# Kernel optimization log

Measured on AMD Instinct MI355X. Metric: run time of the kernel, lower is better.

## Reference

```python
import jax, jax.numpy as jnp
import numpy as np

B = 4
H32, W32 = 10, 32  # x_blocks[-1] spatial size (320x1024 input, stride 32)


def _conv3x3(x, w, b, mode):
    # Conv3x3: explicit pad (zero / reflect / edge==replicate) then VALID 3x3 conv
    if mode == 'zero':
        xp = jnp.pad(x, ((0, 0), (0, 0), (1, 1), (1, 1)))
    else:
        xp = jnp.pad(x, ((0, 0), (0, 0), (1, 1), (1, 1)), mode=mode)
    y = jax.lax.conv_general_dilated(xp, w, (1, 1), 'VALID',
                                     dimension_numbers=('NCHW', 'OIHW', 'NCHW'))
    return y + b[None, :, None, None]


def _maxpool(x, k):
    # nn.MaxPool2d(k, stride=1, padding=k//2)
    return jax.lax.reduce_window(x, -jnp.inf, jax.lax.max,
                                 (1, 1, k, k), (1, 1, 1, 1), 'SAME')


def _up2x(x):
    return jnp.repeat(jnp.repeat(x, 2, axis=2), 2, axis=3)


def _idwt_haar(ll, lh, hl, hh):
    # single-level inverse Haar DWT (orthonormal); pad mode irrelevant for length-2 filters
    b, c, h, w = ll.shape
    x00 = (ll + lh + hl + hh) * 0.5
    x01 = (ll - lh + hl - hh) * 0.5
    x10 = (ll + lh - hl - hh) * 0.5
    x11 = (ll - lh - hl + hh) * 0.5
    top = jnp.stack([x00, x01], axis=4).reshape(b, c, h, 2 * w)
    bot = jnp.stack([x10, x11], axis=4).reshape(b, c, h, 2 * w)
    return jnp.stack([top, bot], axis=3).reshape(b, c, 2 * h, 2 * w)


def _leaky(x):
    return jax.nn.leaky_relu(x, 0.2)


def setup_inputs():
    key = jax.random.key(0)
    ks = jax.random.split(key, 24)
    f = 1104  # int(2208 * 0.5)

    def w(k, o, i):
        return jax.random.normal(k, (o, i, 3, 3), jnp.float32) * (1.0 / np.sqrt(9.0 * i))

    def bs(k, o):
        return jax.random.normal(k, (o,), jnp.float32) * 0.01

    return {
        'x32': jax.random.normal(ks[0], (B, 2208, H32, W32), jnp.float32),
        'x16': jax.random.normal(ks[1], (B, 384, 2 * H32, 2 * W32), jnp.float32),
        'x8': jax.random.normal(ks[2], (B, 192, 4 * H32, 4 * W32), jnp.float32),
        'x4': jax.random.normal(ks[3], (B, 96, 8 * H32, 8 * W32), jnp.float32),
        'conv2_w': w(ks[4], f, 2208), 'conv2_b': bs(ks[5], f),
        'up1_w': w(ks[6], f // 2, f + 384), 'up1_b': bs(ks[7], f // 2),
        'wave1ll_w': w(ks[8], 1, f // 2), 'wave1ll_b': bs(ks[9], 1),
        'wave1_w': w(ks[10], 3, f // 2), 'wave1_b': bs(ks[11], 3),
        'up2_w': w(ks[12], f // 4, f // 2 + 192), 'up2_b': bs(ks[13], f // 4),
        'wave2_w': w(ks[14], 3, f // 4), 'wave2_b': bs(ks[15], 3),
        'up3_w': w(ks[16], f // 8, f // 4 + 96), 'up3_b': bs(ks[17], f // 8),
        'wave3_w': w(ks[18], 3, f // 8), 'wave3_b': bs(ks[19], 3),
    }


def reference(x32, x16, x8, x4, conv2_w, conv2_b, up1_w, up1_b,
              wave1ll_w, wave1ll_b, wave1_w, wave1_b, up2_w, up2_b,
              wave2_w, wave2_b, up3_w, up3_b, wave3_w, wave3_b):
    tr = 0.1  # thresh_ratio default
    # dense stem
    x_d0 = _conv3x3(x32, conv2_w, conv2_b, 'edge')  # replicate pad
    x_d1 = _leaky(_conv3x3(jnp.concatenate([_up2x(x_d0), x16], 1), up1_w, up1_b, 'reflect'))
    ll = 8.0 * _conv3x3(x_d1, wave1ll_w, wave1ll_b, 'edge')   # 2**3 * LL, [B,1,20,64]
    h = 4.0 * _conv3x3(x_d1, wave1_w, wave1_b, 'zero')        # 2**2 * (LH,HL,HH)
    ll = _idwt_haar(ll, h[:, 0:1], h[:, 1:2], h[:, 2:3])       # [B,1,40,128]

    # --- sparse level 1: dense-equivalent gather-compute-scatter via masks ---
    thresh = (ll.max() - ll.min()) * tr
    mask = (jnp.max(jnp.abs(h), axis=1, keepdims=True) > thresh).astype(jnp.float32)
    up_m = (_maxpool(mask, 5) > 0).astype(jnp.float32)
    conva_m = (_maxpool(_up2x(mask), 5) > 0).astype(jnp.float32)
    wave_m = (_maxpool(_up2x(mask), 3) > 0).astype(jnp.float32)
    wavelet_m = _up2x(mask)
    feat = jnp.concatenate([_up2x(x_d1 * up_m), x8], 1) * conva_m
    xa = _leaky(_conv3x3(feat, up2_w, up2_b, 'reflect')) * wave_m
    h = 2.0 * _conv3x3(xa, wave2_w, wave2_b, 'zero') * wavelet_m
    ll = _idwt_haar(ll, h[:, 0:1], h[:, 1:2], h[:, 2:3])       # [B,1,80,256]

    # --- sparse level 0 ---
    thresh = (ll.max() - ll.min()) * tr
    mask = (jnp.max(jnp.abs(h), axis=1, keepdims=True) > thresh).astype(jnp.float32)
    up_m = (_maxpool(mask, 5) > 0).astype(jnp.float32)
    conva_m = (_maxpool(_up2x(mask), 5) > 0).astype(jnp.float32)
    wave_m = (_maxpool(_up2x(mask), 3) > 0).astype(jnp.float32)
    wavelet_m = _up2x(mask)
    feat = jnp.concatenate([_up2x(xa * up_m), x4], 1) * conva_m  # sparse_select + sparse_upsample
    xb = _leaky(_conv3x3(feat, up3_w, up3_b, 'reflect')) * wave_m
    h = _conv3x3(xb, wave3_w, wave3_b, 'zero') * wavelet_m
    ll = _idwt_haar(ll, h[:, 0:1], h[:, 1:2], h[:, 2:3])       # [B,1,160,512]
    return ll  # outputs['disp', 0]
```

## Files before the change

kernel.cpp:

```cpp
#include <hip/hip_runtime.h>
#include <hip/hip_bf16.h>
#include <stdint.h>


typedef float f32x4 __attribute__((ext_vector_type(4)));
typedef short s16x8 __attribute__((ext_vector_type(8)));

__device__ __forceinline__ ushort f2bf(float f) {
    uint32_t u = __float_as_uint(f);
    u += 0x7FFFu + ((u >> 16) & 1u);
    return (ushort)(u >> 16);
}
__device__ __forceinline__ float bf2f(ushort h) {
    return __uint_as_float(((uint32_t)h) << 16);
}

__global__ __launch_bounds__(256)
void repack_w_k(const float* __restrict__ w, ushort* __restrict__ out,
                int OC, int CT, int ICOFF, int CAR, int CAP, int CAT,
                int CBR, int CBP, int SEG, int OCP, int KT)
{
    const int KG = KT / 8;
    const int u = blockIdx.x * 256 + threadIdx.x;
    if (u >= OCP * KG) return;
    const int oc = u / KG, kg = u - oc * KG;
    const int k0 = kg * 8;
    int ic, lo; bool ok;
    if (k0 < SEG * CAP) {
        const int seg = k0 / CAP, c = k0 - seg * CAP;
        lo = (seg == 2); ic = ICOFF + c; ok = (c < CAR);
    } else {
        const int kb = k0 - SEG * CAP;
        const int seg = kb / CBP, c = kb - seg * CBP;
        lo = (seg == 2); ic = CAT + c; ok = (c < CBR);
    }
    ok = ok && (oc < OC);
    for (int t = 0; t < 9; ++t) {
        ushort q[8];
#pragma unroll
        for (int j = 0; j < 8; ++j) q[j] = 0;
        if (ok) {
#pragma unroll
            for (int j = 0; j < 8; ++j) {
                const float v = w[((size_t)oc * CT + ic + j) * 9 + t];
                const ushort h = f2bf(v);
                q[j] = lo ? f2bf(v - bf2f(h)) : h;
            }
        }
        *(uint4*)(out + ((size_t)t * OCP + oc) * KT + k0) = *(uint4*)q;
    }
}

template<bool SPLIT>
__global__ __launch_bounds__(256)
void repack_x_k(const float* __restrict__ in, ushort* __restrict__ out,
                int C, int HW, int OST, int LOOFF)
{
    __shared__ float tile[32][65];
    const int b = blockIdx.z, c0 = blockIdx.y * 32, p0 = blockIdx.x * 64;
    for (int e = threadIdx.x; e < 2048; e += 256) {
        const int cl = e >> 6, pl = e & 63;
        tile[cl][pl] = in[((size_t)b * C + c0 + cl) * HW + p0 + pl];
    }
    __syncthreads();
    const int pl = threadIdx.x >> 2, cg = (threadIdx.x & 3) * 8;
    ushort hv[8], lv[8];
#pragma unroll
    for (int j = 0; j < 8; ++j) {
        const float v = tile[cg + j][pl];
        const ushort h = f2bf(v);
        hv[j] = h;
        lv[j] = f2bf(v - bf2f(h));
    }
    const size_t o = ((size_t)b * HW + p0 + pl) * OST + c0 + cg;
    *(uint4*)(out + o) = *(uint4*)hv;
    if constexpr (SPLIT) *(uint4*)(out + LOOFF + o) = *(uint4*)lv;
}

template<int MODE, int WR, int WC, int WROWS, int WCOLF, int NOCF,
         int H, int W, int OCP, int KT, int CAP, int CBP, int SEG,
         int ASTR, int APLSTR, int AOFF, int CAR, int BSTR, int KS,
         bool SOUT, bool ACCIN>
__global__ __launch_bounds__(256, 1)
void conv_mfma_k(const ushort* __restrict__ xA, const ushort* __restrict__ xB,
                 const ushort* __restrict__ wgt, const float* __restrict__ bias,
                 const float* __restrict__ upm, const float* __restrict__ cam,
                 const float* __restrict__ wvm,
                 ushort* __restrict__ outb, float* __restrict__ outp, int OC)
{
    constexpr int BROWS = WR * WROWS;
    constexpr int NOC = NOCF * 16;
    constexpr int PH = BROWS + 2, PW = 34;
    constexpr int NPX = PH * PW;
    constexpr int ICS = 32;
    constexpr int WRS = 32;
    constexpr int NAU = NPX * 4;
    constexpr int NWU = 9 * NOC * 4;
    constexpr int NSA = (NAU + 255) / 256;
    constexpr int NSW = (NWU + 255) / 256;
    constexpr int NCH = KT / 32;
    constexpr int XT = W / 32;
    constexpr int HP = ((H + BROWS - 1) / BROWS) * BROWS;
    constexpr int HA = (MODE == 0) ? H : H / 2;
    constexpr int WA = (MODE == 0) ? W : W / 2;

    __shared__ __align__(16) ushort atile[NPX * ICS];
    __shared__ __align__(16) ushort wtile[9 * NOC * WRS];

    const int tid = threadIdx.x;
    const int b = blockIdx.z / KS, sid = blockIdx.z % KS;
    const int oc0 = blockIdx.y * NOC;
    const int y0 = (blockIdx.x / XT) * BROWS;
    const int x0 = (blockIdx.x % XT) * 32;
    const int lane = tid & 63, wv = tid >> 6;
    const int wr = wv / WC, wc = wv % WC;
    const int lq = lane >> 4, ln = lane & 15;
    const int wcb = wc * (WCOLF * 16);

    const int c0 = (sid * NCH) / KS, c1 = ((sid + 1) * NCH) / KS;

    int aBA[NSA], aBB[NSA], aLD[NSA], aKO[NSA];
    bool agA[NSA], agB[NSA];
    for (int s = 0; s < NSA; ++s) {
        const int u = tid + s * 256;
        const bool val = u < NAU;
        const int uc = val ? u : 0;
        const int pp = uc >> 2, ug = uc & 3;
        const int py = pp / PW, px = pp - py * PW;
        int y = y0 + py - 1, x = x0 + px - 1;
        if (MODE == 0) { y = min(max(y, 0), H - 1); x = min(max(x, 0), W - 1); }
        else { y = (y < 0) ? -y : ((y >= H) ? 2 * H - 2 - y : y);
               x = (x < 0) ? -x : ((x >= W) ? 2 * W - 2 - x : x); }
        const int ya = (MODE == 0) ? y : (y >> 1);
        const int xa = (MODE == 0) ? x : (x >> 1);
        aBA[s] = ((b * HA + ya) * WA + xa) * ASTR;
        aBB[s] = ((b * H + y) * W + x) * BSTR;
        agA[s] = val; agB[s] = val;
        if (MODE == 2) {
            const float cm = cam[((size_t)b * H + y) * W + x];
            const float um = upm[((size_t)b * HA + ya) * WA + xa];
            agA[s] = agA[s] && (um * cm != 0.f);
            agB[s] = agB[s] && (cm != 0.f);
        }
        aLD[s] = pp * ICS + ((ug ^ ((pp >> 1) & 3)) * 8);
        aKO[s] = ug * 8;
    }
    int wGB[NSW], wLD[NSW]; bool wVv[NSW];
    for (int s = 0; s < NSW; ++s) {
        const int u = tid + s * 256;
        wVv[s] = u < NWU;
        const int uc = wVv[s] ? u : 0;
        const int t = uc / (NOC * 4), r = uc - t * (NOC * 4);
        const int ocl = r >> 2, kg = r & 3;
        const int wrow = t * NOC + ocl;
        wGB[s] = (t * OCP + oc0 + ocl) * KT + kg * 8;
        wLD[s] = wrow * WRS + ((kg ^ ((wrow >> 1) & 3)) * 8);
    }

    uint4 ra[NSA], rw[NSW];
    auto fetch = [&](int kc) {
#pragma unroll
        for (int s = 0; s < NSA; ++s) {
            const int k = kc * 32 + aKO[s];
            uint4 v = {0, 0, 0, 0};
            if (k < SEG * CAP) {
                int ka = (SEG == 3 && k >= 2 * CAP) ? k - 2 * CAP : k;
                const int pl = (ka >= CAP) ? 1 : 0;
                const int c = ka - pl * CAP;
                bool ok = agA[s];
                if (CAR < CAP) ok = ok && (c < CAR);
                if (ok) v = *(const uint4*)(xA + (size_t)aBA[s] + pl * APLSTR + AOFF + c);
            } else {
                int kb = k - SEG * CAP;
                if (SEG == 3 && kb >= 2 * CBP) kb -= 2 * CBP;
                if (agB[s]) v = *(const uint4*)(xB + (size_t)aBB[s] + kb);
            }
            ra[s] = v;
        }
#pragma unroll
        for (int s = 0; s < NSW; ++s) {
            uint4 v = {0, 0, 0, 0};
            if (wVv[s]) v = *(const uint4*)(wgt + (size_t)wGB[s] + kc * 32);
            rw[s] = v;
        }
    };
    auto put = [&]() {
#pragma unroll
        for (int s = 0; s < NSA; ++s)
            if (tid + s * 256 < NAU) *(uint4*)&atile[aLD[s]] = ra[s];
#pragma unroll
        for (int s = 0; s < NSW; ++s)
            if (wVv[s]) *(uint4*)&wtile[wLD[s]] = rw[s];
    };

    f32x4 acc[WROWS][WCOLF][NOCF];
#pragma unroll
    for (int i = 0; i < WROWS; ++i)
#pragma unroll
        for (int c = 0; c < WCOLF; ++c)
#pragma unroll
            for (int n = 0; n < NOCF; ++n) acc[i][c][n] = {0.f, 0.f, 0.f, 0.f};

    if (ACCIN) {
#pragma unroll
        for (int ri = 0; ri < WROWS; ++ri) {
            const float* Pr = outp +
                ((((size_t)sid * 4 + b) * HP + y0 + wr * WROWS + ri) * W + x0 + wcb) * OCP;
#pragma unroll
            for (int cf = 0; cf < WCOLF; ++cf)
#pragma unroll
                for (int n2 = 0; n2 < NOCF; ++n2)
#pragma unroll
                    for (int r = 0; r < 4; ++r)
                        acc[ri][cf][n2][r] =
                            Pr[(size_t)(cf * 16 + lq * 4 + r) * OCP + oc0 + n2 * 16 + ln];
        }
    }

    fetch(c0);
    put();
    __syncthreads();

    for (int kc = c0; kc < c1; ++kc) {
        const bool hn = (kc + 1 < c1);
        if (hn) fetch(kc + 1);
        s16x8 afr[WROWS + 2][WCOLF][3];
#pragma unroll
        for (int ar = 0; ar < WROWS + 2; ++ar)
#pragma unroll
            for (int cf = 0; cf < WCOLF; ++cf)
#pragma unroll
                for (int dx = 0; dx < 3; ++dx) {
                    const int p = (wr * WROWS + ar) * PW + wcb + cf * 16 + ln + dx;
                    afr[ar][cf][dx] = *(const s16x8*)
                        &atile[p * ICS + ((lq ^ ((p >> 1) & 3)) * 8)];
                }
#pragma unroll
        for (int t = 0; t < 9; ++t) {
            const int dy = t / 3, dx = t - dy * 3;
#pragma unroll
            for (int n2 = 0; n2 < NOCF; ++n2) {
                const int wrow = t * NOC + n2 * 16 + ln;
                const s16x8 bw = *(const s16x8*)
                    &wtile[wrow * WRS + ((lq ^ ((wrow >> 1) & 3)) * 8)];
#pragma unroll
                for (int ri = 0; ri < WROWS; ++ri)
#pragma unroll
                    for (int cf = 0; cf < WCOLF; ++cf)
                        acc[ri][cf][n2] = __builtin_amdgcn_mfma_f32_16x16x32_bf16(
                            afr[ri + dy][cf][dx], bw, acc[ri][cf][n2], 0, 0, 0);
            }
        }
        __syncthreads();
        if (hn) { put(); __syncthreads(); }
    }

    if (KS > 1) {
#pragma unroll
        for (int ri = 0; ri < WROWS; ++ri) {
            float* Pr = outp +
                ((((size_t)sid * 4 + b) * HP + y0 + wr * WROWS + ri) * W + x0 + wcb) * OCP;
#pragma unroll
            for (int cf = 0; cf < WCOLF; ++cf)
#pragma unroll
                for (int n2 = 0; n2 < NOCF; ++n2)
#pragma unroll
                    for (int r = 0; r < 4; ++r)
                        Pr[(size_t)(cf * 16 + lq * 4 + r) * OCP + oc0 + n2 * 16 + ln] =
                            acc[ri][cf][n2][r];
        }
    } else {
        constexpr int OST = SOUT ? 2 * OCP : OCP;
#pragma unroll
        for (int ri = 0; ri < WROWS; ++ri) {
            const int y = y0 + wr * WROWS + ri;
#pragma unroll
            for (int cf = 0; cf < WCOLF; ++cf)
#pragma unroll
                for (int n2 = 0; n2 < NOCF; ++n2) {
                    const int oc = oc0 + n2 * 16 + ln;
                    const float bv = (oc < OC) ? bias[oc] : 0.f;
#pragma unroll
                    for (int r = 0; r < 4; ++r) {
                        const int x = x0 + wcb + cf * 16 + lq * 4 + r;
                        float v = acc[ri][cf][n2][r] + bv;
                        v = v > 0.f ? v : 0.2f * v;
                        v *= wvm[((size_t)b * H + y) * W + x];
                        if (oc >= OC) v = 0.f;
                        const size_t o = (((size_t)b * H + y) * W + x) * OST + oc;
                        const ushort h = f2bf(v);
                        outb[o] = h;
                        if constexpr (SOUT) outb[o + OCP] = f2bf(v - bf2f(h));
                    }
                }
        }
    }
}

template<int KS, int HP, int H, int W, int OCP, bool ACT>
__global__ __launch_bounds__(256)
void reduce_k(const float* __restrict__ P, const float* __restrict__ bias,
              ushort* __restrict__ out, int OC)
{
    constexpr int OG = OCP / 4;
    const int u = blockIdx.x * 256 + threadIdx.x;
    if (u >= 4 * H * W * OG) return;
    const int og = u % OG;
    const int px = u / OG;
    const int x = px % W, y = (px / W) % H, b = px / (W * H);
    float4 s = {0.f, 0.f, 0.f, 0.f};
    for (int sid = 0; sid < KS; ++sid) {
        const float4 v = *(const float4*)
            (P + ((((size_t)sid * 4 + b) * HP + y) * W + x) * OCP + og * 4);
        s.x += v.x; s.y += v.y; s.z += v.z; s.w += v.w;
    }
    const int oc = og * 4;
    const float vv[4] = {s.x, s.y, s.z, s.w};
    ushort hi[4], lo[4];
#pragma unroll
    for (int j = 0; j < 4; ++j) {
        float v = (oc + j < OC) ? vv[j] + bias[oc + j] : 0.f;
        if (ACT) v = v > 0.f ? v : 0.2f * v;
        const ushort h = f2bf(v);
        hi[j] = h;
        lo[j] = f2bf(v - bf2f(h));
    }
    const size_t o = (size_t)px * 2 * OCP + oc;
    *(uint2*)(out + o) = *(uint2*)hi;
    *(uint2*)(out + o + OCP) = *(uint2*)lo;
}

__global__ __launch_bounds__(256)
void repack_wv_k(const float* __restrict__ wh, const float* __restrict__ wll,
                 float* __restrict__ out, int C, int CP)
{
    const int u = blockIdx.x * 256 + threadIdx.x;
    if (u >= 9 * CP) return;
    const int t = u / CP, ic = u - t * CP;
    float4 v = {0.f, 0.f, 0.f, 0.f};
    if (ic < C) {
        v.x = wh[((size_t)0 * C + ic) * 9 + t];
        v.y = wh[((size_t)1 * C + ic) * 9 + t];
        v.z = wh[((size_t)2 * C + ic) * 9 + t];
        if (wll) v.w = wll[(size_t)ic * 9 + t];
    }
    *(float4*)(out + (size_t)u * 4) = v;
}

template<int G, int CSTR, int LOOFF, int H, int W, bool SIN, bool HAS_LL>
__global__ __launch_bounds__(256)
void wave_cl_k(const ushort* __restrict__ xq, const float* __restrict__ wv,
               const float* __restrict__ bh, const float* __restrict__ bll,
               const float* __restrict__ mhalf, float scale,
               float* __restrict__ outh, float* __restrict__ outll)
{
    const int lane = threadIdx.x & 63;
    const int pix = blockIdx.x * 4 + (threadIdx.x >> 6);
    const int x = pix % W, y = (pix / W) % H, b = pix / (W * H);
    float a0 = 0.f, a1 = 0.f, a2 = 0.f, a3 = 0.f;
    for (int it = lane; it < 9 * G; it += 64) {
        const int t = it / G, g = it - t * G;
        const int dy = t / 3 - 1, dx = t % 3 - 1;
        const int yy = y + dy, xx = x + dx;
        const int yc = min(max(yy, 0), H - 1), xc = min(max(xx, 0), W - 1);
        const bool inr = (yy >= 0) && (yy < H) && (xx >= 0) && (xx < W);
        const size_t base = (((size_t)b * H + yc) * W + xc) * CSTR + g * 8;
        const uint4 hv = *(const uint4*)(xq + base);
        uint4 lv = {0, 0, 0, 0};
        if constexpr (!SIN) lv = *(const uint4*)(xq + base + LOOFF);
        const float4* wp = (const float4*)(wv + ((size_t)t * (G * 8) + g * 8) * 4);
        const uint* hw = (const uint*)&hv;
        const uint* lw = (const uint*)&lv;
#pragma unroll
        for (int j = 0; j < 8; ++j) {
            const uint wd = hw[j >> 1];
            float xf = (j & 1) ? __uint_as_float(wd & 0xFFFF0000u)
                               : __uint_as_float(wd << 16);
            if constexpr (!SIN) {
                const uint wl = lw[j >> 1];
                xf += (j & 1) ? __uint_as_float(wl & 0xFFFF0000u)
                              : __uint_as_float(wl << 16);
            }
            const float xz = inr ? xf : 0.f;
            const float4 w4 = wp[j];
            a0 = fmaf(w4.x, xz, a0);
            a1 = fmaf(w4.y, xz, a1);
            a2 = fmaf(w4.z, xz, a2);
            if constexpr (HAS_LL) a3 = fmaf(w4.w, xf, a3);
        }
    }
#pragma unroll
    for (int o = 1; o < 64; o <<= 1) {
        a0 += __shfl_xor(a0, o);
        a1 += __shfl_xor(a1, o);
        a2 += __shfl_xor(a2, o);
        if constexpr (HAS_LL) a3 += __shfl_xor(a3, o);
    }
    if (lane == 0) {
        float wm = 1.f;
        if (mhalf) wm = mhalf[((size_t)b * (H / 2) + (y >> 1)) * (W / 2) + (x >> 1)];
        const size_t hb = (size_t)b * 3 * H * W + (size_t)y * W + x;
        outh[hb]             = (a0 + bh[0]) * scale * wm;
        outh[hb + H * W]     = (a1 + bh[1]) * scale * wm;
        outh[hb + 2 * H * W] = (a2 + bh[2]) * scale * wm;
        if constexpr (HAS_LL) outll[((size_t)b * H + y) * W + x] = (a3 + bll[0]) * 8.f;
    }
}

template<int H, int W>
__global__ __launch_bounds__(256)
void idwt_k(const float* __restrict__ ll, const float* __restrict__ h,
            float* __restrict__ out)
{
    const int g = blockIdx.x * 256 + threadIdx.x;
    if (g >= 4 * H * W) return;
    const int x = g % W, y = (g / W) % H, b = g / (W * H);
    const float l  = ll[g];
    const float lh = h[((size_t)(b * 3 + 0) * H + y) * W + x];
    const float hl = h[((size_t)(b * 3 + 1) * H + y) * W + x];
    const float hh = h[((size_t)(b * 3 + 2) * H + y) * W + x];
    const float x00 = (l + lh + hl + hh) * 0.5f;
    const float x01 = (l - lh + hl - hh) * 0.5f;
    const float x10 = (l + lh - hl - hh) * 0.5f;
    const float x11 = (l - lh - hl + hh) * 0.5f;
    float* ob = out + (size_t)b * (2 * H) * (2 * W);
    ob[(size_t)(2 * y) * (2 * W) + 2 * x]         = x00;
    ob[(size_t)(2 * y) * (2 * W) + 2 * x + 1]     = x01;
    ob[(size_t)(2 * y + 1) * (2 * W) + 2 * x]     = x10;
    ob[(size_t)(2 * y + 1) * (2 * W) + 2 * x + 1] = x11;
}

__global__ __launch_bounds__(256)
void minmax_k(const float* __restrict__ p, int n, float* __restrict__ thr)
{
    __shared__ float smax[256], smin[256];
    float mx = -1e30f, mn = 1e30f;
    for (int i = threadIdx.x; i < n; i += 256) {
        const float v = p[i];
        mx = fmaxf(mx, v);
        mn = fminf(mn, v);
    }
    smax[threadIdx.x] = mx;
    smin[threadIdx.x] = mn;
    __syncthreads();
    for (int s = 128; s > 0; s >>= 1) {
        if (threadIdx.x < s) {
            smax[threadIdx.x] = fmaxf(smax[threadIdx.x], smax[threadIdx.x + s]);
            smin[threadIdx.x] = fminf(smin[threadIdx.x], smin[threadIdx.x + s]);
        }
        __syncthreads();
    }
    if (threadIdx.x == 0) *thr = (smax[0] - smin[0]) * 0.1f;
}

template<int H, int W>
__global__ __launch_bounds__(256)
void mask_k(const float* __restrict__ h, const float* __restrict__ thr,
            float* __restrict__ mask)
{
    const int g = blockIdx.x * 256 + threadIdx.x;
    if (g >= 4 * H * W) return;
    const int x = g % W, y = (g / W) % H, b = g / (W * H);
    const float t  = *thr;
    const float v0 = fabsf(h[((size_t)(b * 3 + 0) * H + y) * W + x]);
    const float v1 = fabsf(h[((size_t)(b * 3 + 1) * H + y) * W + x]);
    const float v2 = fabsf(h[((size_t)(b * 3 + 2) * H + y) * W + x]);
    mask[g] = (fmaxf(v0, fmaxf(v1, v2)) > t) ? 1.f : 0.f;
}

template<int H, int W, int R>
__global__ __launch_bounds__(256)
void dilate_k(const float* __restrict__ m, float* __restrict__ o)
{
    const int g = blockIdx.x * 256 + threadIdx.x;
    if (g >= 4 * H * W) return;
    const int x = g % W, y = (g / W) % H, b = g / (W * H);
    float v = 0.f;
    for (int dy = -R; dy <= R; ++dy) {
        const int yy = y + dy;
        if (yy < 0 || yy >= H) continue;
        for (int dx = -R; dx <= R; ++dx) {
            const int xx = x + dx;
            if (xx < 0 || xx >= W) continue;
            v = fmaxf(v, m[((size_t)b * H + yy) * W + xx]);
        }
    }
    o[g] = (v > 0.f) ? 1.f : 0.f;
}

template<int H, int W>
__global__ __launch_bounds__(256)
void masksfull_k(const float* __restrict__ m, float* __restrict__ conva,
                 float* __restrict__ wavem)
{
    const int g = blockIdx.x * 256 + threadIdx.x;
    constexpr int H2 = 2 * H, W2 = 2 * W;
    if (g >= 4 * H2 * W2) return;
    const int x = g % W2, y = (g / W2) % H2, b = g / (W2 * H2);
    float c5 = 0.f, c3 = 0.f;
    for (int dy = -2; dy <= 2; ++dy) {
        const int yy = y + dy;
        if (yy < 0 || yy >= H2) continue;
        const int my = yy >> 1;
        for (int dx = -2; dx <= 2; ++dx) {
            const int xx = x + dx;
            if (xx < 0 || xx >= W2) continue;
            const float v = m[((size_t)b * H + my) * W + (xx >> 1)];
            c5 = fmaxf(c5, v);
            if (dy >= -1 && dy <= 1 && dx >= -1 && dx <= 1) c3 = fmaxf(c3, v);
        }
    }
    conva[g] = (c5 > 0.f) ? 1.f : 0.f;
    wavem[g] = (c3 > 0.f) ? 1.f : 0.f;
}

static constexpr size_t WSTEM = 0;
static constexpr size_t WUP1  = 0;
static constexpr size_t X16   = 46780416ull;
static constexpr size_t WUP2  = 54644736ull;
static constexpr size_t XB    = 0ull;
static constexpr size_t X4    = 23592960ull;
static constexpr size_t WUP3  = 66769920ull;
static constexpr size_t WV1   = 67765248ull;
static constexpr size_t WV2   = 67844736ull;
static constexpr size_t WV3   = 67885056ull;
static constexpr size_t X32   = 66769920ull;
static constexpr size_t XD0   = 78074880ull;
static constexpr size_t PF    = 83727360ull;
static constexpr size_t XAOF  = 83727360ull;
static constexpr size_t XD1   = 110859264ull;
static constexpr size_t X8    = 122655744ull;
static constexpr size_t F32B  = 138384384ull;
static constexpr size_t O_LL1 = 0, O_H1 = 5120, O_LLB = 20480, O_H2 = 40960;
static constexpr size_t O_LLC = 102400, O_H3 = 184320, O_M1 = 430080;
static constexpr size_t O_UPM1 = 435200, O_CAM1 = 440320, O_WM1 = 460800;
static constexpr size_t O_M2 = 481280, O_UPM2 = 501760, O_CAM2 = 522240;
static constexpr size_t O_WM2 = 604160, O_RED = 686080;

extern "C" void kernel_launch(void* const* d_in, const int* in_sizes, int n_in,
                              void* d_out, int out_size, void* d_ws, size_t ws_size,
                              hipStream_t stream)
{
    const float* x32     = (const float*)d_in[0];
    const float* x16     = (const float*)d_in[1];
    const float* x8      = (const float*)d_in[2];
    const float* x4      = (const float*)d_in[3];
    const float* conv2_w = (const float*)d_in[4];
    const float* conv2_b = (const float*)d_in[5];
    const float* up1_w   = (const float*)d_in[6];
    const float* up1_b   = (const float*)d_in[7];
    const float* w1ll_w  = (const float*)d_in[8];
    const float* w1ll_b  = (const float*)d_in[9];
    const float* w1_w    = (const float*)d_in[10];
    const float* w1_b    = (const float*)d_in[11];
    const float* up2_w   = (const float*)d_in[12];
    const float* up2_b   = (const float*)d_in[13];
    const float* w2_w    = (const float*)d_in[14];
    const float* w2_b    = (const float*)d_in[15];
    const float* up3_w   = (const float*)d_in[16];
    const float* up3_b   = (const float*)d_in[17];
    const float* w3_w    = (const float*)d_in[18];
    const float* w3_b    = (const float*)d_in[19];

    char* ws = (char*)d_ws;
    auto U = [&](size_t off) { return (ushort*)(ws + off); };
    float* Pf  = (float*)(ws + PF);
    float* f32 = (float*)(ws + F32B);
    float* ll1   = f32 + O_LL1;
    float* h1    = f32 + O_H1;
    float* llb   = f32 + O_LLB;
    float* h2    = f32 + O_H2;
    float* llc   = f32 + O_LLC;
    float* h3    = f32 + O_H3;
    float* mask1 = f32 + O_M1;
    float* upm1  = f32 + O_UPM1;
    float* cam1  = f32 + O_CAM1;
    float* wm1   = f32 + O_WM1;
    float* mask2 = f32 + O_M2;
    float* upm2  = f32 + O_UPM2;
    float* cam2  = f32 + O_CAM2;
    float* wm2   = f32 + O_WM2;
    float* wv1   = (float*)(ws + WV1);
    float* wv2   = (float*)(ws + WV2);
    float* wv3   = (float*)(ws + WV3);

    repack_x_k<true><<<dim3(5, 69, 4), 256, 0, stream>>>(x32, U(X32), 2208, 320, 4416, 2208);
    repack_w_k<<<1812, 256, 0, stream>>>(conv2_w, U(WSTEM), 1104, 2208, 0, 1104, 1120, 0, 0, 8, 3, 1104, 3360);
    conv_mfma_k<0, 2, 2, 2, 1, 3, 10, 32, 1104, 3360, 1120, 8, 3, 4416, 2208, 0, 1104, 1, 4, false, false>
        <<<dim3(3, 23, 16), 256, 0, stream>>>(U(X32), nullptr, U(WSTEM), nullptr,
            nullptr, nullptr, nullptr, nullptr, Pf, 1104);
    repack_w_k<<<1812, 256, 0, stream>>>(conv2_w, U(WSTEM), 1104, 2208, 1104, 1104, 1120, 0, 0, 8, 3, 1104, 3360);
    conv_mfma_k<0, 2, 2, 2, 1, 3, 10, 32, 1104, 3360, 1120, 8, 3, 4416, 2208, 1104, 1104, 1, 4, false, true>
        <<<dim3(3, 23, 16), 256, 0, stream>>>(U(X32), nullptr, U(WSTEM), nullptr,
            nullptr, nullptr, nullptr, nullptr, Pf, 1104);
    reduce_k<4, 12, 10, 32, 1104, false><<<1380, 256, 0, stream>>>(Pf, conv2_b, U(XD0), 1104);
    repack_w_k<<<1269, 256, 0, stream>>>(up1_w, U(WUP1), 552, 1488, 0, 1104, 1120, 1104, 384, 384, 3, 576, 4512);
    repack_x_k<true><<<dim3(20, 12, 4), 256, 0, stream>>>(x16, U(X16), 384, 1280, 768, 384);
    repack_w_k<<<324, 256, 0, stream>>>(up2_w, U(WUP2), 276, 744, 0, 552, 576, 552, 192, 192, 3, 288, 2304);
    repack_w_k<<<27, 256, 0, stream>>>(up3_w, U(WUP3), 138, 372, 0, 276, 288, 276, 96, 96, 1, 144, 384);
    repack_x_k<true><<<dim3(80, 6, 4), 256, 0, stream>>>(x8, U(X8), 192, 5120, 384, 192);
    repack_wv_k<<<20, 256, 0, stream>>>(w1_w, w1ll_w, wv1, 552, 552);
    repack_wv_k<<<10, 256, 0, stream>>>(w2_w, nullptr, wv2, 276, 280);
    repack_wv_k<<<6, 256, 0, stream>>>(w3_w, nullptr, wv3, 138, 144);
    conv_mfma_k<1, 2, 2, 2, 1, 4, 20, 64, 576, 4512, 1120, 384, 3, 2208, 1104, 0, 1104, 768, 2, false, false>
        <<<dim3(10, 9, 8), 256, 0, stream>>>(U(XD0), U(X16), U(WUP1), nullptr,
            nullptr, nullptr, nullptr, nullptr, Pf, 552);
    reduce_k<2, 20, 20, 64, 576, true><<<2880, 256, 0, stream>>>(Pf, up1_b, U(XD1), 552);
    repack_x_k<false><<<dim3(320, 3, 4), 256, 0, stream>>>(x4, U(X4), 96, 20480, 96, 0);
    wave_cl_k<69, 1152, 576, 20, 64, false, true><<<1280, 256, 0, stream>>>(
        U(XD1), wv1, w1_b, w1ll_b, nullptr, 4.f, h1, ll1);
    idwt_k<20, 64><<<20, 256, 0, stream>>>(ll1, h1, llb);
    minmax_k<<<1, 256, 0, stream>>>(llb, 20480, f32 + O_RED);
    mask_k<20, 64><<<20, 256, 0, stream>>>(h1, f32 + O_RED, mask1);
    dilate_k<20, 64, 2><<<20, 256, 0, stream>>>(mask1, upm1);
    masksfull_k<20, 64><<<80, 256, 0, stream>>>(mask1, cam1, wm1);
    conv_mfma_k<2, 4, 1, 2, 2, 3, 40, 128, 288, 2304, 576, 192, 3, 1152, 576, 0, 576, 384, 1, true, false>
        <<<dim3(20, 6, 4), 256, 0, stream>>>(U(XD1), U(X8), U(WUP2), up2_b,
            upm1, cam1, wm1, U(XAOF), nullptr, 276);
    wave_cl_k<35, 576, 288, 40, 128, false, false><<<5120, 256, 0, stream>>>(
        U(XAOF), wv2, w2_b, nullptr, mask1, 2.f, h2, nullptr);
    idwt_k<40, 128><<<80, 256, 0, stream>>>(llb, h2, llc);
    minmax_k<<<1, 256, 0, stream>>>(llc, 81920, f32 + O_RED + 1);
    mask_k<40, 128><<<80, 256, 0, stream>>>(h2, f32 + O_RED + 1, mask2);
    dilate_k<40, 128, 2><<<80, 256, 0, stream>>>(mask2, upm2);
    masksfull_k<40, 128><<<320, 256, 0, stream>>>(mask2, cam2, wm2);
    conv_mfma_k<2, 4, 1, 2, 2, 3, 80, 256, 144, 384, 288, 96, 1, 576, 288, 0, 288, 96, 1, false, false>
        <<<dim3(80, 3, 4), 256, 0, stream>>>(U(XAOF), U(X4), U(WUP3), up3_b,
            upm2, cam2, wm2, U(XB), nullptr, 138);
    wave_cl_k<18, 144, 0, 80, 256, true, false><<<20480, 256, 0, stream>>>(
        U(XB), wv3, w3_b, nullptr, mask2, 1.f, h3, nullptr);
    idwt_k<80, 256><<<320, 256, 0, stream>>>(llc, h3, (float*)d_out);
}
```

Baseline: 2.558 ms.

## Double-buffer conv tiles with direct global-to-LDS async loads and retiled blocks

Replaces the register-staged fetch/put loop of the MFMA conv kernel with global_load_lds direct-to-LDS copies into two LDS buffers, so the next K-chunk loads while the current one computes and one barrier per iteration is dropped. Masked or out-of-range loads are redirected to a zeroed pad buffer instead of predicated zero writes, which needs a new zeroing kernel and a workspace shift. Block tiling, OC-per-block and launch bounds (2 blocks/CU) are retuned for each conv. The risk is LDS pressure and the lost CAR channel check, which now relies on zero-padded data, for example in the XD0 head.

After: 2.639 ms. +3.1%, slower.

```diff
diff --git a/kernel.cpp b/kernel.cpp
--- a/kernel.cpp
+++ b/kernel.cpp
@@ -5,6 +5,13 @@
 
 typedef float f32x4 __attribute__((ext_vector_type(4)));
 typedef short s16x8 __attribute__((ext_vector_type(8)));
+
+typedef const __attribute__((address_space(1))) void* gas_ptr;
+typedef __attribute__((address_space(3))) void* las_ptr;
+
+__device__ __forceinline__ void gl_lds16(const void* g, void* l) {
+    __builtin_amdgcn_global_load_lds((gas_ptr)g, (las_ptr)l, 16, 0, 0);
+}
 
 __device__ __forceinline__ ushort f2bf(float f) {
     uint32_t u = __float_as_uint(f);
@@ -13,6 +20,15 @@
 }
 __device__ __forceinline__ float bf2f(ushort h) {
     return __uint_as_float(((uint32_t)h) << 16);
+}
+
+__global__ __launch_bounds__(256)
+void zero_k(ushort* __restrict__ zp, ushort* __restrict__ xd0head)
+{
+    const int t = threadIdx.x;
+    const uint4 z = {0, 0, 0, 0};
+    for (int i = t; i < 1024; i += 256) *(uint4*)(zp + i * 8) = z;
+    if (t < 16) *(uint4*)(xd0head + t * 8) = z;
 }
 
 __global__ __launch_bounds__(256)
@@ -79,118 +95,109 @@
 
 template<int MODE, int WR, int WC, int WROWS, int WCOLF, int NOCF,
          int H, int W, int OCP, int KT, int CAP, int CBP, int SEG,
-         int ASTR, int APLSTR, int AOFF, int CAR, int BSTR, int KS,
+         int ASTR, int APLSTR, int AOFF, int BSTR, int KS,
          bool SOUT, bool ACCIN>
-__global__ __launch_bounds__(256, 1)
-void conv_mfma_k(const ushort* __restrict__ xA, const ushort* __restrict__ xB,
-                 const ushort* __restrict__ wgt, const float* __restrict__ bias,
-                 const float* __restrict__ upm, const float* __restrict__ cam,
-                 const float* __restrict__ wvm,
-                 ushort* __restrict__ outb, float* __restrict__ outp, int OC)
+__global__ __launch_bounds__(256, 2)
+void conv_async_k(const ushort* __restrict__ xA, const ushort* __restrict__ xB,
+                  const ushort* __restrict__ wgt, const float* __restrict__ bias,
+                  const float* __restrict__ upm, const float* __restrict__ cam,
+                  const float* __restrict__ wvm, const ushort* __restrict__ zpad,
+                  ushort* __restrict__ outb, float* __restrict__ outp, int OC)
 {
     constexpr int BROWS = WR * WROWS;
+    constexpr int BCOLS = WC * WCOLF * 16;
     constexpr int NOC = NOCF * 16;
-    constexpr int PH = BROWS + 2, PW = 34;
+    constexpr int PH = BROWS + 2, PW = BCOLS + 2;
     constexpr int NPX = PH * PW;
-    constexpr int ICS = 32;
-    constexpr int WRS = 32;
     constexpr int NAU = NPX * 4;
+    constexpr int ASL = ((NAU + 63) / 64) * 64;
     constexpr int NWU = 9 * NOC * 4;
-    constexpr int NSA = (NAU + 255) / 256;
+    constexpr int NSA = (ASL + 255) / 256;
     constexpr int NSW = (NWU + 255) / 256;
+    constexpr int PERBUF = (ASL + NWU) * 8;
     constexpr int NCH = KT / 32;
-    constexpr int XT = W / 32;
+    constexpr int XT = W / BCOLS;
     constexpr int HP = ((H + BROWS - 1) / BROWS) * BROWS;
     constexpr int HA = (MODE == 0) ? H : H / 2;
     constexpr int WA = (MODE == 0) ? W : W / 2;
-
-    __shared__ __align__(16) ushort atile[NPX * ICS];
-    __shared__ __align__(16) ushort wtile[9 * NOC * WRS];
+    constexpr bool HASB = (SEG * CAP < KT);
+
+    __shared__ __align__(16) ushort lds[2 * PERBUF];
 
     const int tid = threadIdx.x;
     const int b = blockIdx.z / KS, sid = blockIdx.z % KS;
     const int oc0 = blockIdx.y * NOC;
     const int y0 = (blockIdx.x / XT) * BROWS;
-    const int x0 = (blockIdx.x % XT) * 32;
+    const int x0 = (blockIdx.x % XT) * BCOLS;
     const int lane = tid & 63, wv = tid >> 6;
     const int wr = wv / WC, wc = wv % WC;
     const int lq = lane >> 4, ln = lane & 15;
     const int wcb = wc * (WCOLF * 16);
-
     const int c0 = (sid * NCH) / KS, c1 = ((sid + 1) * NCH) / KS;
-
-    int aBA[NSA], aBB[NSA], aLD[NSA], aKO[NSA];
-    bool agA[NSA], agB[NSA];
+    const int wbv = wv * 512;
+
+    const ushort* pAp[NSA]; const ushort* pBp[NSA]; int aKO[NSA];
     for (int s = 0; s < NSA; ++s) {
         const int u = tid + s * 256;
-        const bool val = u < NAU;
-        const int uc = val ? u : 0;
-        const int pp = uc >> 2, ug = uc & 3;
-        const int py = pp / PW, px = pp - py * PW;
+        const int pp = u >> 2, sl = u & 3;
+        aKO[s] = (sl ^ ((pp >> 1) & 3)) * 8;
+        const bool val = pp < NPX;
+        const int ppc = val ? pp : 0;
+        const int py = ppc / PW, px = ppc - py * PW;
         int y = y0 + py - 1, x = x0 + px - 1;
         if (MODE == 0) { y = min(max(y, 0), H - 1); x = min(max(x, 0), W - 1); }
         else { y = (y < 0) ? -y : ((y >= H) ? 2 * H - 2 - y : y);
                x = (x < 0) ? -x : ((x >= W) ? 2 * W - 2 - x : x); }
         const int ya = (MODE == 0) ? y : (y >> 1);
         const int xa = (MODE == 0) ? x : (x >> 1);
-        aBA[s] = ((b * HA + ya) * WA + xa) * ASTR;
-        aBB[s] = ((b * H + y) * W + x) * BSTR;
-        agA[s] = val; agB[s] = val;
+        bool okA = val, okB = val;
         if (MODE == 2) {
             const float cm = cam[((size_t)b * H + y) * W + x];
             const float um = upm[((size_t)b * HA + ya) * WA + xa];
-            agA[s] = agA[s] && (um * cm != 0.f);
-            agB[s] = agB[s] && (cm != 0.f);
-        }
-        aLD[s] = pp * ICS + ((ug ^ ((pp >> 1) & 3)) * 8);
-        aKO[s] = ug * 8;
-    }
-    int wGB[NSW], wLD[NSW]; bool wVv[NSW];
+            okA = okA && (um * cm != 0.f);
+            okB = okB && (cm != 0.f);
+        }
+        pAp[s] = okA ? xA + (size_t)((b * HA + ya) * WA + xa) * ASTR : zpad;
+        if constexpr (HASB)
+            pBp[s] = okB ? xB + (size_t)((b * H + y) * W + x) * BSTR : zpad;
+        else
+            pBp[s] = zpad;
+    }
+    const ushort* pWp[NSW];
     for (int s = 0; s < NSW; ++s) {
         const int u = tid + s * 256;
-        wVv[s] = u < NWU;
-        const int uc = wVv[s] ? u : 0;
-        const int t = uc / (NOC * 4), r = uc - t * (NOC * 4);
-        const int ocl = r >> 2, kg = r & 3;
-        const int wrow = t * NOC + ocl;
-        wGB[s] = (t * OCP + oc0 + ocl) * KT + kg * 8;
-        wLD[s] = wrow * WRS + ((kg ^ ((wrow >> 1) & 3)) * 8);
-    }
-
-    uint4 ra[NSA], rw[NSW];
-    auto fetch = [&](int kc) {
+        const int wrow = u >> 2, sl = u & 3;
+        const int kg = sl ^ ((wrow >> 1) & 3);
+        const int t = wrow / NOC, ocl = wrow - t * NOC;
+        pWp[s] = (u < NWU) ?
+            wgt + (size_t)(t * OCP + oc0 + ocl) * KT + kg * 8 : zpad;
+    }
+
+    auto stage = [&](int buf, int kc) {
+        ushort* ab = lds + buf * PERBUF;
+        ushort* wb = ab + ASL * 8;
+        const int ko = kc * 32;
 #pragma unroll
         for (int s = 0; s < NSA; ++s) {
-            const int k = kc * 32 + aKO[s];
-            uint4 v = {0, 0, 0, 0};
-            if (k < SEG * CAP) {
-                int ka = (SEG == 3 && k >= 2 * CAP) ? k - 2 * CAP : k;
-                const int pl = (ka >= CAP) ? 1 : 0;
-                const int c = ka - pl * CAP;
-                bool ok = agA[s];
-                if (CAR < CAP) ok = ok && (c < CAR);
-                if (ok) v = *(const uint4*)(xA + (size_t)aBA[s] + pl * APLSTR + AOFF + c);
-            } else {
-                int kb = k - SEG * CAP;
-                if (SEG == 3 && kb >= 2 * CBP) kb -= 2 * CBP;
-                if (agB[s]) v = *(const uint4*)(xB + (size_t)aBB[s] + kb);
+            if (s * 256 + wv * 64 < NAU) {
+                const int k = ko + aKO[s];
+                const ushort* g;
+                if (!HASB || k < SEG * CAP) {
+                    int ka = (SEG == 3 && k >= 2 * CAP) ? k - 2 * CAP : k;
+                    const int pl = (ka >= CAP) ? 1 : 0;
+                    g = pAp[s] + pl * APLSTR + AOFF + (ka - pl * CAP);
+                } else {
+                    int kb = k - SEG * CAP;
+                    if (SEG == 3 && kb >= 2 * CBP) kb -= 2 * CBP;
+                    g = pBp[s] + kb;
+                }
+                gl_lds16(g, ab + s * 2048 + wbv);
             }
-            ra[s] = v;
-        }
-#pragma unroll
-        for (int s = 0; s < NSW; ++s) {
-            uint4 v = {0, 0, 0, 0};
-            if (wVv[s]) v = *(const uint4*)(wgt + (size_t)wGB[s] + kc * 32);
-            rw[s] = v;
-        }
-    };
-    auto put = [&]() {
-#pragma unroll
-        for (int s = 0; s < NSA; ++s)
-            if (tid + s * 256 < NAU) *(uint4*)&atile[aLD[s]] = ra[s];
+        }
 #pragma unroll
         for (int s = 0; s < NSW; ++s)
-            if (wVv[s]) *(uint4*)&wtile[wLD[s]] = rw[s];
+            if (s * 256 + wv * 64 < NWU)
+                gl_lds16(pWp[s] + ko, wb + s * 2048 + wbv);
     };
 
     f32x4 acc[WROWS][WCOLF][NOCF];
@@ -217,13 +224,13 @@
         }
     }
 
-    fetch(c0);
-    put();
+    stage(0, c0);
     __syncthreads();
-
+    int cur = 0;
     for (int kc = c0; kc < c1; ++kc) {
-        const bool hn = (kc + 1 < c1);
-        if (hn) fetch(kc + 1);
+        if (kc + 1 < c1) stage(cur ^ 1, kc + 1);
+        const ushort* at = lds + cur * PERBUF;
+        const ushort* wt = at + ASL * 8;
         s16x8 afr[WROWS + 2][WCOLF][3];
 #pragma unroll
         for (int ar = 0; ar < WROWS + 2; ++ar)
@@ -233,7 +240,7 @@
                 for (int dx = 0; dx < 3; ++dx) {
                     const int p = (wr * WROWS + ar) * PW + wcb + cf * 16 + ln + dx;
                     afr[ar][cf][dx] = *(const s16x8*)
-                        &atile[p * ICS + ((lq ^ ((p >> 1) & 3)) * 8)];
+                        &at[p * 32 + ((lq ^ ((p >> 1) & 3)) * 8)];
                 }
 #pragma unroll
         for (int t = 0; t < 9; ++t) {
@@ -242,7 +249,7 @@
             for (int n2 = 0; n2 < NOCF; ++n2) {
                 const int wrow = t * NOC + n2 * 16 + ln;
                 const s16x8 bw = *(const s16x8*)
-                    &wtile[wrow * WRS + ((lq ^ ((wrow >> 1) & 3)) * 8)];
+                    &wt[wrow * 32 + ((lq ^ ((wrow >> 1) & 3)) * 8)];
 #pragma unroll
                 for (int ri = 0; ri < WROWS; ++ri)
 #pragma unroll
@@ -252,7 +259,7 @@
             }
         }
         __syncthreads();
-        if (hn) { put(); __syncthreads(); }
+        cur ^= 1;
     }
 
     if (KS > 1) {
@@ -526,8 +533,9 @@
 static constexpr size_t WV3   = 67885056ull;
 static constexpr size_t X32   = 66769920ull;
 static constexpr size_t XD0   = 78074880ull;
-static constexpr size_t PF    = 83727360ull;
-static constexpr size_t XAOF  = 83727360ull;
+static constexpr size_t ZPADO = 83727360ull;
+static constexpr size_t PF    = 83743744ull;
+static constexpr size_t XAOF  = 83743744ull;
 static constexpr size_t XD1   = 110859264ull;
 static constexpr size_t X8    = 122655744ull;
 static constexpr size_t F32B  = 138384384ull;
@@ -583,16 +591,19 @@
     float* wv1   = (float*)(ws + WV1);
     float* wv2   = (float*)(ws + WV2);
     float* wv3   = (float*)(ws + WV3);
+    const ushort* zp = U(ZPADO);
+
+    zero_k<<<1, 256, 0, stream>>>(U(ZPADO), U(XD0));
 
     repack_x_k<true><<<dim3(5, 69, 4), 256, 0, stream>>>(x32, U(X32), 2208, 320, 4416, 2208);
     repack_w_k<<<1812, 256, 0, stream>>>(conv2_w, U(WSTEM), 1104, 2208, 0, 1104, 1120, 0, 0, 8, 3, 1104, 3360);
-    conv_mfma_k<0, 2, 2, 2, 1, 3, 10, 32, 1104, 3360, 1120, 8, 3, 4416, 2208, 0, 1104, 1, 4, false, false>
-        <<<dim3(3, 23, 16), 256, 0, stream>>>(U(X32), nullptr, U(WSTEM), nullptr,
-            nullptr, nullptr, nullptr, nullptr, Pf, 1104);
+    conv_async_k<0, 4, 1, 1, 1, 3, 10, 32, 1104, 3360, 1120, 8, 3, 4416, 2208, 0, 1, 4, false, false>
+        <<<dim3(6, 23, 16), 256, 0, stream>>>(U(X32), nullptr, U(WSTEM), nullptr,
+            nullptr, nullptr, nullptr, zp, nullptr, Pf, 1104);
     repack_w_k<<<1812, 256, 0, stream>>>(conv2_w, U(WSTEM), 1104, 2208, 1104, 1104, 1120, 0, 0, 8, 3, 1104, 3360);
-    conv_mfma_k<0, 2, 2, 2, 1, 3, 10, 32, 1104, 3360, 1120, 8, 3, 4416, 2208, 1104, 1104, 1, 4, false, true>
-        <<<dim3(3, 23, 16), 256, 0, stream>>>(U(X32), nullptr, U(WSTEM), nullptr,
-            nullptr, nullptr, nullptr, nullptr, Pf, 1104);
+    conv_async_k<0, 4, 1, 1, 1, 3, 10, 32, 1104, 3360, 1120, 8, 3, 4416, 2208, 1104, 1, 4, false, true>
+        <<<dim3(6, 23, 16), 256, 0, stream>>>(U(X32), nullptr, U(WSTEM), nullptr,
+            nullptr, nullptr, nullptr, zp, nullptr, Pf, 1104);
     reduce_k<4, 12, 10, 32, 1104, false><<<1380, 256, 0, stream>>>(Pf, conv2_b, U(XD0), 1104);
     repack_w_k<<<1269, 256, 0, stream>>>(up1_w, U(WUP1), 552, 1488, 0, 1104, 1120, 1104, 384, 384, 3, 576, 4512);
     repack_x_k<true><<<dim3(20, 12, 4), 256, 0, stream>>>(x16, U(X16), 384, 1280, 768, 384);
@@ -602,9 +613,9 @@
     repack_wv_k<<<20, 256, 0, stream>>>(w1_w, w1ll_w, wv1, 552, 552);
     repack_wv_k<<<10, 256, 0, stream>>>(w2_w, nullptr, wv2, 276, 280);
     repack_wv_k<<<6, 256, 0, stream>>>(w3_w, nullptr, wv3, 138, 144);
-    conv_mfma_k<1, 2, 2, 2, 1, 4, 20, 64, 576, 4512, 1120, 384, 3, 2208, 1104, 0, 1104, 768, 2, false, false>
-        <<<dim3(10, 9, 8), 256, 0, stream>>>(U(XD0), U(X16), U(WUP1), nullptr,
-            nullptr, nullptr, nullptr, nullptr, Pf, 552);
+    conv_async_k<1, 2, 2, 2, 1, 2, 20, 64, 576, 4512, 1120, 384, 3, 2208, 1104, 0, 768, 2, false, false>
+        <<<dim3(10, 18, 8), 256, 0, stream>>>(U(XD0), U(X16), U(WUP1), nullptr,
+            nullptr, nullptr, nullptr, zp, nullptr, Pf, 552);
     reduce_k<2, 20, 20, 64, 576, true><<<2880, 256, 0, stream>>>(Pf, up1_b, U(XD1), 552);
     repack_x_k<false><<<dim3(320, 3, 4), 256, 0, stream>>>(x4, U(X4), 96, 20480, 96, 0);
     wave_cl_k<69, 1152, 576, 20, 64, false, true><<<1280, 256, 0, stream>>>(
@@ -614,9 +625,9 @@
     mask_k<20, 64><<<20, 256, 0, stream>>>(h1, f32 + O_RED, mask1);
     dilate_k<20, 64, 2><<<20, 256, 0, stream>>>(mask1, upm1);
     masksfull_k<20, 64><<<80, 256, 0, stream>>>(mask1, cam1, wm1);
-    conv_mfma_k<2, 4, 1, 2, 2, 3, 40, 128, 288, 2304, 576, 192, 3, 1152, 576, 0, 576, 384, 1, true, false>
-        <<<dim3(20, 6, 4), 256, 0, stream>>>(U(XD1), U(X8), U(WUP2), up2_b,
-            upm1, cam1, wm1, U(XAOF), nullptr, 276);
+    conv_async_k<2, 2, 2, 2, 1, 2, 40, 128, 288, 2304, 576, 192, 3, 1152, 576, 0, 384, 1, true, false>
+        <<<dim3(40, 9, 4), 256, 0, stream>>>(U(XD1), U(X8), U(WUP2), up2_b,
+            upm1, cam1, wm1, zp, U(XAOF), nullptr, 276);
     wave_cl_k<35, 576, 288, 40, 128, false, false><<<5120, 256, 0, stream>>>(
         U(XAOF), wv2, w2_b, nullptr, mask1, 2.f, h2, nullptr);
     idwt_k<40, 128><<<80, 256, 0, stream>>>(llb, h2, llc);
@@ -624,9 +635,9 @@
     mask_k<40, 128><<<80, 256, 0, stream>>>(h2, f32 + O_RED + 1, mask2);
     dilate_k<40, 128, 2><<<80, 256, 0, stream>>>(mask2, upm2);
     masksfull_k<40, 128><<<320, 256, 0, stream>>>(mask2, cam2, wm2);
-    conv_mfma_k<2, 4, 1, 2, 2, 3, 80, 256, 144, 384, 288, 96, 1, 576, 288, 0, 288, 96, 1, false, false>
-        <<<dim3(80, 3, 4), 256, 0, stream>>>(U(XAOF), U(X4), U(WUP3), up3_b,
-            upm2, cam2, wm2, U(XB), nullptr, 138);
+    conv_async_k<2, 2, 2, 2, 1, 1, 80, 256, 144, 384, 288, 96, 1, 576, 288, 0, 96, 1, false, false>
+        <<<dim3(160, 9, 4), 256, 0, stream>>>(U(XAOF), U(X4), U(WUP3), up3_b,
+            upm2, cam2, wm2, zp, U(XB), nullptr, 138);
     wave_cl_k<18, 144, 0, 80, 256, true, false><<<20480, 256, 0, stream>>>(
         U(XB), wv3, w3_b, nullptr, mask2, 1.f, h3, nullptr);
     idwt_k<80, 256><<<320, 256, 0, stream>>>(llc, h3, (float*)d_out);
```
